# Kernel optimization log

Measured on AMD Instinct MI355X. Metric: run time of the kernel, lower is better.

The kernel has to match this reference:

```python
import jax, jax.numpy as jnp
import numpy as np

B, D, S, H, L = 256, 7, 32, 512, 128  # batch, tree depth, n_symbols, hidden_size, latent_size
N = 2 ** D - 1  # nodes in complete binary tree, heap order (children of i are 2i+1, 2i+2)


def _xavier(key, shape):
    lim = float(np.sqrt(6.0 / (shape[0] + shape[1])))
    return jax.random.uniform(key, shape, jnp.float32, -lim, lim)


def setup_inputs():
    key = jax.random.key(0)
    ks = jax.random.split(key, 18)
    return {
        'symbols': jax.random.randint(ks[0], (B, N), 0, S, dtype=jnp.int32),
        'eps': jax.random.normal(ks[1], (B, L), jnp.float32),
        # Encoder GRU221: gate order [r, z, n], input weights act on one-hot symbol, hidden weights on cat(h_l, h_r)
        'ewi': _xavier(ks[2], (3 * H, S)),
        'ebi': jax.random.uniform(ks[3], (3 * H,), jnp.float32, -0.05, 0.05),
        'ewh': _xavier(ks[4], (3 * H, 2 * H)),
        'ebh': jax.random.uniform(ks[5], (3 * H,), jnp.float32, -0.05, 0.05),
        'h2mu_w': _xavier(ks[6], (L, H)),
        'h2mu_b': jax.random.uniform(ks[7], (L,), jnp.float32, -0.05, 0.05),
        'h2lv_w': _xavier(ks[8], (L, H)),
        'h2lv_b': jax.random.uniform(ks[9], (L,), jnp.float32, -0.05, 0.05),
        # Decoder
        'z2h_w': _xavier(ks[10], (H, L)),
        'z2h_b': jax.random.uniform(ks[11], (H,), jnp.float32, -0.05, 0.05),
        'h2o_w': _xavier(ks[12], (S, H)),
        'h2o_b': jax.random.uniform(ks[13], (S,), jnp.float32, -0.05, 0.05),
        # Decoder GRU122: gate order [r, z, n], each gate has 2H outputs (left/right child)
        'dwi': _xavier(ks[14], (6 * H, S)),
        'dbi': jax.random.uniform(ks[15], (6 * H,), jnp.float32, -0.05, 0.05),
        'dwh': _xavier(ks[16], (6 * H, H)),
        'dbh': jax.random.uniform(ks[17], (6 * H,), jnp.float32, -0.05, 0.05),
    }


def _hvae_forward(symbols, eps, ewi, ebi, ewh, ebh, h2mu_w, h2mu_b, h2lv_w, h2lv_b,
                  z2h_w, z2h_b, h2o_w, h2o_b, dwi, dbi, dwh, dbh):
    x_all = jax.nn.one_hot(symbols, S, dtype=jnp.float32)  # [B, N, S] node targets

    # ---- Encoder: GRU221 applied bottom-up, one batched step per tree level ----
    h = jnp.zeros((B, 2 ** D, H), jnp.float32)  # (absent) children of the deepest level
    for d in range(D - 1, -1, -1):
        n_d = 2 ** d
        x = x_all[:, n_d - 1: 2 * n_d - 1]       # [B, n_d, S] level-d symbols (heap order)
        hl, hr = h[:, 0::2], h[:, 1::2]           # [B, n_d, H] left/right child hiddens
        hcat = jnp.concatenate([hl, hr], axis=-1)
        gi = x @ ewi.T + ebi                       # [B, n_d, 3H]
        gh = hcat @ ewh.T + ebh
        r = jax.nn.sigmoid(gi[..., :H] + gh[..., :H])
        zg = jax.nn.sigmoid(gi[..., H:2 * H] + gh[..., H:2 * H])
        n = jnp.tanh(gi[..., 2 * H:] + r * gh[..., 2 * H:])
        h = (1.0 - zg) * n + zg * (hl + hr) * 0.5
    root = h[:, 0]                                 # [B, H]
    mu = root @ h2mu_w.T + h2mu_b                  # [B, L]
    logvar = root @ h2lv_w.T + h2lv_b
    zlat = mu + eps * jnp.exp(0.5 * logvar)        # reparameterized sample

    # ---- Decoder: GRU122 applied top-down, one batched step per tree level ----
    hidden = (zlat @ z2h_w.T + z2h_b)[:, None, :]  # [B, 1, H] root hidden
    preds = []
    for d in range(D):
        pred = hidden @ h2o_w.T + h2o_b            # [B, 2^d, S]
        preds.append(pred)
        if d < D - 1:
            a = jax.nn.softmax(pred, axis=-1)
            gi = a @ dwi.T + dbi                    # [B, 2^d, 6H]
            gh = hidden @ dwh.T + dbh
            r = jax.nn.sigmoid(gi[..., :2 * H] + gh[..., :2 * H])
            zg = jax.nn.sigmoid(gi[..., 2 * H:4 * H] + gh[..., 2 * H:4 * H])
            n = jnp.tanh(gi[..., 4 * H:] + r * gh[..., 4 * H:])
            dh = jnp.concatenate([hidden, hidden], axis=-1)  # h.repeat(1,1,2)
            out = (1.0 - zg) * n + zg * dh          # [B, 2^d, 2H]
            # torch.split -> (left, right); interleave as next level's hiddens (heap order)
            hidden = jnp.stack([out[..., :H], out[..., H:]], axis=2).reshape(B, 2 ** (d + 1), H)
    preds = jnp.concatenate(preds, axis=1)          # [B, N, S] per-node logits, level order
    return mu, logvar, preds


def reference(symbols, eps, ewi, ebi, ewh, ebh, h2mu_w, h2mu_b, h2lv_w, h2lv_b,
              z2h_w, z2h_b, h2o_w, h2o_b, dwi, dbi, dwh, dbh):
    return _hvae_forward(symbols, eps, ewi, ebi, ewh, ebh, h2mu_w, h2mu_b, h2lv_w, h2lv_b,
                         z2h_w, z2h_b, h2o_w, h2o_b, dwi, dbi, dwh, dbh)
```

## Files before the change

kernel.cpp:

```cpp
#include <hip/hip_runtime.h>
#include <hip/hip_bf16.h>

typedef unsigned short u16;
typedef unsigned int u32;
typedef __attribute__((ext_vector_type(8))) short short8;
typedef __attribute__((ext_vector_type(4))) float f32x4;

#define WAITV(N) asm volatile("s_waitcnt vmcnt(" #N ")" ::: "memory")

__device__ __forceinline__ float sigmoidf_(float x) { return 1.0f / (1.0f + expf(-x)); }
__device__ __forceinline__ float fsig(float x) {
    return __builtin_amdgcn_rcpf(1.0f + __expf(-x));
}
__device__ __forceinline__ float ftanh(float x) {
    x = fminf(fmaxf(x, -15.0f), 15.0f);
    float t = __expf(2.0f * x);
    return (t - 1.0f) * __builtin_amdgcn_rcpf(t + 1.0f);
}

__device__ __forceinline__ float bf2f(u16 u) {
    union { u32 i; float f; } v; v.i = ((u32)u) << 16; return v.f;
}
__device__ __forceinline__ u16 f2bf(float f) {
    union { float f; u32 i; } v; v.f = f;
    u32 lsb = (v.i >> 16) & 1u;
    v.i += 0x7fffu + lsb;
    return (u16)(v.i >> 16);
}

__device__ __forceinline__ void gload16(const u16* g, u16* l) {
    __builtin_amdgcn_global_load_lds(
        (const __attribute__((address_space(1))) u32*)g,
        (__attribute__((address_space(3))) u32*)l, 16, 0, 0);
}

__global__ __launch_bounds__(256) void prep(
    const float* __restrict__ ewh, const float* __restrict__ dwh,
    const float* __restrict__ dwi, const float* __restrict__ ewi,
    const float* __restrict__ h2o_w, const int* __restrict__ symbols,
    const float* __restrict__ ebi, const float* __restrict__ ebh,
    u16* __restrict__ ewh_b, u16* __restrict__ dwh_b, u16* __restrict__ dwi_b,
    u16* __restrict__ ewi_b, u16* __restrict__ wo_b, u16* __restrict__ oneh,
    u16* __restrict__ ltab)
{
    int idx = blockIdx.x * 256 + threadIdx.x;
    if (idx < 1572864) { ewh_b[idx] = f2bf(ewh[idx]); return; }
    idx -= 1572864;
    if (idx < 1572864) { dwh_b[idx] = f2bf(dwh[idx]); return; }
    idx -= 1572864;
    if (idx < 98304) { dwi_b[idx] = f2bf(dwi[idx]); return; }
    idx -= 98304;
    if (idx < 49152) { ewi_b[idx] = f2bf(ewi[idx]); return; }
    idx -= 49152;
    if (idx < 16384) { wo_b[idx] = f2bf(h2o_w[idx]); return; }
    idx -= 16384;
    if (idx < 1040384) {
        int col = idx & 31, row = idx >> 5;
        oneh[idx] = (col == symbols[row]) ? (u16)0x3F80 : (u16)0;
        return;
    }
    idx -= 1040384;
    if (idx < 16384) {
        int c = idx & 511, sym = idx >> 9;
        float r = sigmoidf_(ewi[c * 32 + sym]          + ebi[c]        + ebh[c]);
        float z = sigmoidf_(ewi[(512 + c) * 32 + sym]  + ebi[512 + c]  + ebh[512 + c]);
        float n = tanhf(    ewi[(1024 + c) * 32 + sym] + ebi[1024 + c] + r * ebh[1024 + c]);
        ltab[idx] = f2bf((1.0f - z) * n);
    }
}

template<int RF, bool LEAF>
__global__ __launch_bounds__(256, 2) void enc_tile(
    const u16* __restrict__ A, const u16* __restrict__ W,
    const u16* __restrict__ oneh, const u16* __restrict__ Wi,
    const u16* __restrict__ tab, const int* __restrict__ symbols,
    const float* __restrict__ ebi, const float* __restrict__ ebh,
    u16* __restrict__ hout, int dlog, int node_base)
{
    constexpr int BM = RF * 32;
    constexpr int NCA = BM / 64;
    constexpr int NS = 32;
    __shared__ alignas(16) u16 Als[2][BM * 32];
    __shared__ alignas(16) u16 Bls[2][192 * 32];
    const int tid  = threadIdx.x;
    const int lane = tid & 63;
    const int wid  = tid >> 6;
    const int wr = wid >> 1, wc = wid & 1;
    const int lr = lane & 15, lk = lane >> 4;
    const int m0 = blockIdx.x * BM;
    const int c0 = blockIdx.y * 64;
    const int mask = (1 << dlog) - 1;

    size_t a_goff[NCA]; int a_loff[NCA];
    int symL[NCA], symR[NCA];
#pragma unroll
    for (int j = 0; j < NCA; ++j) {
        int a = wid * NCA + j;
        int r_ = a * 16 + (lane >> 2);
        int kps = (lane & 3) ^ ((r_ >> 1) & 3);
        a_loff[j] = a * 512 + lane * 8;
        if constexpr (LEAF) {
            int rg = m0 + r_;
            int b_ = rg >> dlog, jj = rg & mask;
            int cbase = b_ * 127 + 2 * (node_base + jj) + 1;
            symL[j] = symbols[cbase];
            symR[j] = symbols[cbase + 1];
            a_goff[j] = kps * 8;
        } else {
            a_goff[j] = (size_t)(m0 + r_) * 1024 + kps * 8;
            symL[j] = symR[j] = 0;
        }
    }
    size_t b_goff[3]; int b_loff[3];
#pragma unroll
    for (int j = 0; j < 3; ++j) {
        int b = wid * 3 + j;
        int rr = b * 16 + (lane >> 2);
        int kps = (lane & 3) ^ ((rr >> 1) & 3);
        int grow = (rr >> 6) * 512 + c0 + (rr & 63);
        b_goff[j] = (size_t)grow * 1024 + kps * 8;
        b_loff[j] = b * 512 + lane * 8;
    }
    int a_roff[RF];
#pragma unroll
    for (int i = 0; i < RF; ++i) {
        int row = wr * (RF * 16) + i * 16 + lr;
        a_roff[i] = row * 32 + (lk ^ ((row >> 1) & 3)) * 8;
    }
    int b_roff[3][2];
#pragma unroll
    for (int s = 0; s < 3; ++s)
#pragma unroll
        for (int cf = 0; cf < 2; ++cf) {
            int row = s * 64 + wc * 32 + cf * 16 + lr;
            b_roff[s][cf] = row * 32 + (lk ^ ((row >> 1) & 3)) * 8;
        }

    f32x4 acc[4][2][RF];
#pragma unroll
    for (int s = 0; s < 4; ++s)
#pragma unroll
        for (int cf = 0; cf < 2; ++cf)
#pragma unroll
            for (int i = 0; i < RF; ++i) acc[s][cf][i] = (f32x4){0.f, 0.f, 0.f, 0.f};

    auto issue = [&](int stg) {
        const int buf = stg & 1;
        const int nk = stg * 32;
#pragma unroll
        for (int j = 0; j < NCA; ++j) {
            if constexpr (LEAF) {
                const u16* src = (nk < 512)
                    ? tab + (size_t)symL[j] * 512 + nk + a_goff[j]
                    : tab + (size_t)symR[j] * 512 + (nk - 512) + a_goff[j];
                gload16(src, &Als[buf][a_loff[j]]);
            } else {
                gload16(A + a_goff[j] + nk, &Als[buf][a_loff[j]]);
            }
        }
#pragma unroll
        for (int j = 0; j < 3; ++j) gload16(W + b_goff[j] + nk, &Bls[buf][b_loff[j]]);
    };
    auto compute = [&](int buf) {
        short8 a[RF];
#pragma unroll
        for (int i = 0; i < RF; ++i)
            a[i] = *reinterpret_cast<const short8*>(&Als[buf][a_roff[i]]);
#pragma unroll
        for (int s = 0; s < 3; ++s)
#pragma unroll
            for (int cf = 0; cf < 2; ++cf) {
                short8 b = *reinterpret_cast<const short8*>(&Bls[buf][b_roff[s][cf]]);
#pragma unroll
                for (int i = 0; i < RF; ++i)
                    acc[s][cf][i] = __builtin_amdgcn_mfma_f32_16x16x32_bf16(b, a[i], acc[s][cf][i], 0, 0, 0);
            }
    };

    issue(0);
    WAITV(0);
    __builtin_amdgcn_s_barrier();
    for (int t = 0; t < NS - 1; ++t) {
        issue(t + 1);
        compute(t & 1);
        WAITV(0);
        __builtin_amdgcn_s_barrier();
    }
    compute((NS - 1) & 1);

    {
        short8 oh[RF];
#pragma unroll
        for (int i = 0; i < RF; ++i) {
            int m = m0 + wr * (RF * 16) + i * 16 + lr;
            int b_ = m >> dlog, j_ = m & mask;
            oh[i] = *reinterpret_cast<const short8*>(
                oneh + (size_t)(b_ * 127 + node_base + j_) * 32 + lk * 8);
        }
#pragma unroll
        for (int s = 0; s < 3; ++s) {
            const int d = (s == 2) ? 3 : s;
#pragma unroll
            for (int cf = 0; cf < 2; ++cf) {
                short8 wb = *reinterpret_cast<const short8*>(
                    Wi + (size_t)(s * 512 + c0 + wc * 32 + cf * 16 + lr) * 32 + lk * 8);
#pragma unroll
                for (int i = 0; i < RF; ++i)
                    acc[d][cf][i] = __builtin_amdgcn_mfma_f32_16x16x32_bf16(wb, oh[i], acc[d][cf][i], 0, 0, 0);
            }
        }
    }

    float4 ebr4[2], ebz4[2], ebin4[2], ebhn4[2];
    int cb[2];
#pragma unroll
    for (int cf = 0; cf < 2; ++cf) {
        cb[cf] = c0 + wc * 32 + cf * 16 + lk * 4;
        float4 bi0 = *reinterpret_cast<const float4*>(ebi + cb[cf]);
        float4 bh0 = *reinterpret_cast<const float4*>(ebh + cb[cf]);
        float4 bi1 = *reinterpret_cast<const float4*>(ebi + 512 + cb[cf]);
        float4 bh1 = *reinterpret_cast<const float4*>(ebh + 512 + cb[cf]);
        ebr4[cf] = make_float4(bi0.x + bh0.x, bi0.y + bh0.y, bi0.z + bh0.z, bi0.w + bh0.w);
        ebz4[cf] = make_float4(bi1.x + bh1.x, bi1.y + bh1.y, bi1.z + bh1.z, bi1.w + bh1.w);
        ebin4[cf] = *reinterpret_cast<const float4*>(ebi + 1024 + cb[cf]);
        ebhn4[cf] = *reinterpret_cast<const float4*>(ebh + 1024 + cb[cf]);
    }
#pragma unroll
    for (int i = 0; i < RF; ++i) {
        int m = m0 + wr * (RF * 16) + i * 16 + lr;
        int symLm = 0, symRm = 0;
        if constexpr (LEAF) {
            int b_ = m >> dlog, jj = m & mask;
            int cbase_ = b_ * 127 + 2 * (node_base + jj) + 1;
            symLm = symbols[cbase_];
            symRm = symbols[cbase_ + 1];
        }
#pragma unroll
        for (int cf = 0; cf < 2; ++cf) {
            ushort4 hl4, hr4;
            if constexpr (LEAF) {
                hl4 = *reinterpret_cast<const ushort4*>(tab + (size_t)symLm * 512 + cb[cf]);
                hr4 = *reinterpret_cast<const ushort4*>(tab + (size_t)symRm * 512 + cb[cf]);
            } else {
                hl4 = *reinterpret_cast<const ushort4*>(A + (size_t)m * 1024 + cb[cf]);
                hr4 = *reinterpret_cast<const ushort4*>(A + (size_t)m * 1024 + 512 + cb[cf]);
            }
            const float eb_r[4] = {ebr4[cf].x, ebr4[cf].y, ebr4[cf].z, ebr4[cf].w};
            const float eb_z[4] = {ebz4[cf].x, ebz4[cf].y, ebz4[cf].z, ebz4[cf].w};
            const float eb_in[4] = {ebin4[cf].x, ebin4[cf].y, ebin4[cf].z, ebin4[cf].w};
            const float eb_hn[4] = {ebhn4[cf].x, ebhn4[cf].y, ebhn4[cf].z, ebhn4[cf].w};
            const u16 hlv[4] = {hl4.x, hl4.y, hl4.z, hl4.w};
            const u16 hrv[4] = {hr4.x, hr4.y, hr4.z, hr4.w};
            ushort4 outv;
            u16* ov = reinterpret_cast<u16*>(&outv);
#pragma unroll
            for (int r = 0; r < 4; ++r) {
                float rr_ = fsig(acc[0][cf][i][r] + eb_r[r]);
                float zz  = fsig(acc[1][cf][i][r] + eb_z[r]);
                float nn  = ftanh(acc[3][cf][i][r] + eb_in[r] + rr_ * (acc[2][cf][i][r] + eb_hn[r]));
                float hm = (bf2f(hlv[r]) + bf2f(hrv[r])) * 0.5f;
                ov[r] = f2bf((1.0f - zz) * nn + zz * hm);
            }
            *reinterpret_cast<ushort4*>(hout + (size_t)m * 512 + cb[cf]) = outv;
        }
    }
}

__global__ __launch_bounds__(256) void midf(
    const u16* __restrict__ root, const float* __restrict__ h2mu_w,
    const float* __restrict__ h2mu_b, const float* __restrict__ h2lv_w,
    const float* __restrict__ h2lv_b, const float* __restrict__ eps,
    const float* __restrict__ z2h_w, const float* __restrict__ z2h_b,
    float* __restrict__ out_mu, float* __restrict__ out_lv,
    u16* __restrict__ hidden)
{
    int b = blockIdx.x, t = threadIdx.x;
    __shared__ float rs[512];
    __shared__ float zl[128];
    rs[t]       = bf2f(root[(size_t)b * 512 + t]);
    rs[t + 256] = bf2f(root[(size_t)b * 512 + t + 256]);
    __syncthreads();
    const float* w = (t < 128) ? (h2mu_w + (size_t)t * 512) : (h2lv_w + (size_t)(t - 128) * 512);
    float acc = 0.0f;
    for (int k = 0; k < 512; ++k) acc += rs[k] * w[k];
    acc += (t < 128) ? h2mu_b[t] : h2lv_b[t - 128];
    __shared__ float vals[256];
    vals[t] = acc;
    __syncthreads();
    if (t < 128) {
        float mu = vals[t], lv = vals[t + 128];
        zl[t] = mu + eps[b * 128 + t] * expf(0.5f * lv);
        out_mu[b * 128 + t] = mu;
        out_lv[b * 128 + t] = lv;
    }
    __syncthreads();
    for (int c = t; c < 512; c += 256) {
        float a2 = z2h_b[c];
        const float* wz = z2h_w + (size_t)c * 128;
        for (int k = 0; k < 128; ++k) a2 += zl[k] * wz[k];
        hidden[(size_t)b * 512 + c] = f2bf(a2);
    }
}

__global__ __launch_bounds__(256) void pred_mfma(
    const u16* __restrict__ hidden, const u16* __restrict__ Wo,
    const float* __restrict__ h2o_b, float* __restrict__ preds_out,
    int dlog, int node_base)
{
    const int lane = threadIdx.x & 63;
    const int wid  = threadIdx.x >> 6;
    const int lr = lane & 15, lk = lane >> 4;
    const int m0 = blockIdx.x * 64 + wid * 16;

    f32x4 acc0 = (f32x4){0.f, 0.f, 0.f, 0.f};
    f32x4 acc1 = (f32x4){0.f, 0.f, 0.f, 0.f};
    const u16* Arow = hidden + (size_t)(m0 + lr) * 512 + lk * 8;
    const u16* B0 = Wo + (size_t)lr * 512 + lk * 8;
    const u16* B1 = Wo + (size_t)(16 + lr) * 512 + lk * 8;
#pragma unroll
    for (int k0 = 0; k0 < 512; k0 += 32) {
        short8 a  = *reinterpret_cast<const short8*>(Arow + k0);
        short8 b0 = *reinterpret_cast<const short8*>(B0 + k0);
        short8 b1 = *reinterpret_cast<const short8*>(B1 + k0);
        acc0 = __builtin_amdgcn_mfma_f32_16x16x32_bf16(b0, a, acc0, 0, 0, 0);
        acc1 = __builtin_amdgcn_mfma_f32_16x16x32_bf16(b1, a, acc1, 0, 0, 0);
    }
    float4 bb0 = *reinterpret_cast<const float4*>(h2o_b + lk * 4);
    float4 bb1 = *reinterpret_cast<const float4*>(h2o_b + 16 + lk * 4);
    float p0[4], p1[4];
    p0[0] = acc0[0] + bb0.x; p0[1] = acc0[1] + bb0.y; p0[2] = acc0[2] + bb0.z; p0[3] = acc0[3] + bb0.w;
    p1[0] = acc1[0] + bb1.x; p1[1] = acc1[1] + bb1.y; p1[2] = acc1[2] + bb1.z; p1[3] = acc1[3] + bb1.w;
    int m = m0 + lr;
    int b_ = m >> dlog, j_ = m & ((1 << dlog) - 1);
    size_t o = (size_t)(b_ * 127 + node_base + j_) * 32;
    *reinterpret_cast<float4*>(preds_out + o + lk * 4)      = make_float4(p0[0], p0[1], p0[2], p0[3]);
    *reinterpret_cast<float4*>(preds_out + o + 16 + lk * 4) = make_float4(p1[0], p1[1], p1[2], p1[3]);
}

template<int RF>
__global__ __launch_bounds__(256, 2) void dec_tile(
    const u16* __restrict__ Hin, const u16* __restrict__ Wh,
    const u16* __restrict__ Wi, const u16* __restrict__ Wo,
    const float* __restrict__ dbh, const float* __restrict__ dbi,
    const float* __restrict__ h2o_b, u16* __restrict__ Hout,
    float* __restrict__ preds_out, int dlog, int node_base)
{
    constexpr int BM = RF * 32;
    constexpr int NCA = BM / 64;
    constexpr int NS = 16;
    __shared__ alignas(16) u16 Als[2][BM * 32];
    __shared__ alignas(16) u16 Bls[2][192 * 32];
    const int tid  = threadIdx.x;
    const int lane = tid & 63;
    const int wid  = tid >> 6;
    const int wr = wid >> 1, wc = wid & 1;
    const int lr = lane & 15, lk = lane >> 4;
    const int m0 = blockIdx.x * BM;
    const int c0 = blockIdx.y * 64;
    const int mask = (1 << dlog) - 1;

    size_t a_goff[NCA]; int a_loff[NCA];
#pragma unroll
    for (int j = 0; j < NCA; ++j) {
        int a = wid * NCA + j;
        int r_ = a * 16 + (lane >> 2);
        int kps = (lane & 3) ^ ((r_ >> 1) & 3);
        a_goff[j] = (size_t)(m0 + r_) * 512 + kps * 8;
        a_loff[j] = a * 512 + lane * 8;
    }
    size_t b_goff[3]; int b_loff[3];
#pragma unroll
    for (int j = 0; j < 3; ++j) {
        int b = wid * 3 + j;
        int rr = b * 16 + (lane >> 2);
        int kps = (lane & 3) ^ ((rr >> 1) & 3);
        int grow = (rr >> 6) * 1024 + c0 + (rr & 63);
        b_goff[j] = (size_t)grow * 512 + kps * 8;
        b_loff[j] = b * 512 + lane * 8;
    }
    int a_roff[RF];
#pragma unroll
    for (int i = 0; i < RF; ++i) {
        int row = wr * (RF * 16) + i * 16 + lr;
        a_roff[i] = row * 32 + (lk ^ ((row >> 1) & 3)) * 8;
    }
    int b_roff[3][2];
#pragma unroll
    for (int s = 0; s < 3; ++s)
#pragma unroll
        for (int cf = 0; cf < 2; ++cf) {
            int row = s * 64 + wc * 32 + cf * 16 + lr;
            b_roff[s][cf] = row * 32 + (lk ^ ((row >> 1) & 3)) * 8;
        }

    f32x4 acc[4][2][RF];
#pragma unroll
    for (int s = 0; s < 4; ++s)
#pragma unroll
        for (int cf = 0; cf < 2; ++cf)
#pragma unroll
            for (int i = 0; i < RF; ++i) acc[s][cf][i] = (f32x4){0.f, 0.f, 0.f, 0.f};
    f32x4 accp[2][RF];
#pragma unroll
    for (int cf = 0; cf < 2; ++cf)
#pragma unroll
        for (int i = 0; i < RF; ++i) accp[cf][i] = (f32x4){0.f, 0.f, 0.f, 0.f};

    auto issue = [&](int stg) {
        const int buf = stg & 1;
        const int nk = stg * 32;
#pragma unroll
        for (int j = 0; j < NCA; ++j) gload16(Hin + a_goff[j] + nk, &Als[buf][a_loff[j]]);
#pragma unroll
        for (int j = 0; j < 3; ++j) gload16(Wh + b_goff[j] + nk, &Bls[buf][b_loff[j]]);
    };
    auto compute = [&](int buf, int t) {
        short8 a[RF];
#pragma unroll
        for (int i = 0; i < RF; ++i)
            a[i] = *reinterpret_cast<const short8*>(&Als[buf][a_roff[i]]);
#pragma unroll
        for (int s = 0; s < 3; ++s)
#pragma unroll
            for (int cf = 0; cf < 2; ++cf) {
                short8 b = *reinterpret_cast<const short8*>(&Bls[buf][b_roff[s][cf]]);
#pragma unroll
                for (int i = 0; i < RF; ++i)
                    acc[s][cf][i] = __builtin_amdgcn_mfma_f32_16x16x32_bf16(b, a[i], acc[s][cf][i], 0, 0, 0);
            }
#pragma unroll
        for (int cf = 0; cf < 2; ++cf) {
            short8 wo = *reinterpret_cast<const short8*>(
                Wo + (size_t)(cf * 16 + lr) * 512 + t * 32 + lk * 8);
#pragma unroll
            for (int i = 0; i < RF; ++i)
                accp[cf][i] = __builtin_amdgcn_mfma_f32_16x16x32_bf16(wo, a[i], accp[cf][i], 0, 0, 0);
        }
    };

    issue(0);
    WAITV(0);
    __builtin_amdgcn_s_barrier();
    for (int t = 0; t < NS - 1; ++t) {
        issue(t + 1);
        compute(t & 1, t);
        WAITV(0);
        __builtin_amdgcn_s_barrier();
    }
    compute((NS - 1) & 1, NS - 1);

    u16* aLds = &Als[0][0];
    {
        float4 bb0 = *reinterpret_cast<const float4*>(h2o_b + lk * 4);
        float4 bb1 = *reinterpret_cast<const float4*>(h2o_b + 16 + lk * 4);
#pragma unroll
        for (int i = 0; i < RF; ++i) {
            float p0[4], p1[4];
            p0[0] = accp[0][i][0] + bb0.x; p0[1] = accp[0][i][1] + bb0.y;
            p0[2] = accp[0][i][2] + bb0.z; p0[3] = accp[0][i][3] + bb0.w;
            p1[0] = accp[1][i][0] + bb1.x; p1[1] = accp[1][i][1] + bb1.y;
            p1[2] = accp[1][i][2] + bb1.z; p1[3] = accp[1][i][3] + bb1.w;
            float mx = fmaxf(fmaxf(fmaxf(p0[0], p0[1]), fmaxf(p0[2], p0[3])),
                             fmaxf(fmaxf(p1[0], p1[1]), fmaxf(p1[2], p1[3])));
            mx = fmaxf(mx, __shfl_xor(mx, 16));
            mx = fmaxf(mx, __shfl_xor(mx, 32));
            float e0[4], e1[4], s = 0.0f;
#pragma unroll
            for (int r = 0; r < 4; ++r) {
                e0[r] = __expf(p0[r] - mx); e1[r] = __expf(p1[r] - mx);
                s += e0[r] + e1[r];
            }
            s += __shfl_xor(s, 16);
            s += __shfl_xor(s, 32);
            int mloc = wr * (RF * 16) + i * 16 + lr;
            int m = m0 + mloc;
            if (blockIdx.y == 0 && wc == 0) {
                int b_ = m >> dlog, j_ = m & mask;
                size_t o = (size_t)(b_ * 127 + node_base + j_) * 32;
                *reinterpret_cast<float4*>(preds_out + o + lk * 4)      = make_float4(p0[0], p0[1], p0[2], p0[3]);
                *reinterpret_cast<float4*>(preds_out + o + 16 + lk * 4) = make_float4(p1[0], p1[1], p1[2], p1[3]);
            }
            if (wc == 0) {
                float inv = __builtin_amdgcn_rcpf(s);
                ushort4 a0, a1;
                u16* av0 = reinterpret_cast<u16*>(&a0);
                u16* av1 = reinterpret_cast<u16*>(&a1);
#pragma unroll
                for (int r = 0; r < 4; ++r) { av0[r] = f2bf(e0[r] * inv); av1[r] = f2bf(e1[r] * inv); }
                *reinterpret_cast<ushort4*>(aLds + mloc * 32 + lk * 4)      = a0;
                *reinterpret_cast<ushort4*>(aLds + mloc * 32 + 16 + lk * 4) = a1;
            }
        }
    }
    __builtin_amdgcn_s_barrier();

#pragma unroll
    for (int i = 0; i < RF; ++i) {
        int mloc = wr * (RF * 16) + i * 16 + lr;
        short8 aw = *reinterpret_cast<const short8*>(aLds + mloc * 32 + lk * 8);
#pragma unroll
        for (int s = 0; s < 3; ++s) {
            const int d = (s == 2) ? 3 : s;
#pragma unroll
            for (int cf = 0; cf < 2; ++cf) {
                short8 b = *reinterpret_cast<const short8*>(
                    Wi + (size_t)(s * 1024 + c0 + wc * 32 + cf * 16 + lr) * 32 + lk * 8);
                acc[d][cf][i] = __builtin_amdgcn_mfma_f32_16x16x32_bf16(b, aw, acc[d][cf][i], 0, 0, 0);
            }
        }
    }

    float4 br4[2], bz4[2], bin4[2], bhn4[2];
    int cb[2];
#pragma unroll
    for (int cf = 0; cf < 2; ++cf) {
        cb[cf] = c0 + wc * 32 + cf * 16 + lk * 4;
        float4 h0 = *reinterpret_cast<const float4*>(dbh + cb[cf]);
        float4 i0 = *reinterpret_cast<const float4*>(dbi + cb[cf]);
        float4 h1 = *reinterpret_cast<const float4*>(dbh + 1024 + cb[cf]);
        float4 i1 = *reinterpret_cast<const float4*>(dbi + 1024 + cb[cf]);
        br4[cf] = make_float4(h0.x + i0.x, h0.y + i0.y, h0.z + i0.z, h0.w + i0.w);
        bz4[cf] = make_float4(h1.x + i1.x, h1.y + i1.y, h1.z + i1.z, h1.w + i1.w);
        bin4[cf] = *reinterpret_cast<const float4*>(dbi + 2048 + cb[cf]);
        bhn4[cf] = *reinterpret_cast<const float4*>(dbh + 2048 + cb[cf]);
    }
#pragma unroll
    for (int i = 0; i < RF; ++i) {
        int m = m0 + wr * (RF * 16) + i * 16 + lr;
#pragma unroll
        for (int cf = 0; cf < 2; ++cf) {
            ushort4 hid4 = *reinterpret_cast<const ushort4*>(Hin + (size_t)m * 512 + (cb[cf] & 511));
            const float b_r[4] = {br4[cf].x, br4[cf].y, br4[cf].z, br4[cf].w};
            const float b_z[4] = {bz4[cf].x, bz4[cf].y, bz4[cf].z, bz4[cf].w};
            const float b_in[4] = {bin4[cf].x, bin4[cf].y, bin4[cf].z, bin4[cf].w};
            const float b_hn[4] = {bhn4[cf].x, bhn4[cf].y, bhn4[cf].z, bhn4[cf].w};
            const u16 hv[4] = {hid4.x, hid4.y, hid4.z, hid4.w};
            ushort4 outv;
            u16* ov = reinterpret_cast<u16*>(&outv);
#pragma unroll
            for (int r = 0; r < 4; ++r) {
                float rr_ = fsig(acc[0][cf][i][r] + b_r[r]);
                float zz  = fsig(acc[1][cf][i][r] + b_z[r]);
                float nn  = ftanh(acc[3][cf][i][r] + b_in[r] + rr_ * (acc[2][cf][i][r] + b_hn[r]));
                ov[r] = f2bf((1.0f - zz) * nn + zz * bf2f(hv[r]));
            }
            *reinterpret_cast<ushort4*>(Hout + (size_t)m * 1024 + cb[cf]) = outv;
        }
    }
}

extern "C" void kernel_launch(void* const* d_in, const int* in_sizes, int n_in,
                              void* d_out, int out_size, void* d_ws, size_t ws_size,
                              hipStream_t stream) {
    const int*   symbols = (const int*)  d_in[0];
    const float* eps     = (const float*)d_in[1];
    const float* ewi     = (const float*)d_in[2];
    const float* ebi     = (const float*)d_in[3];
    const float* ewh     = (const float*)d_in[4];
    const float* ebh     = (const float*)d_in[5];
    const float* h2mu_w  = (const float*)d_in[6];
    const float* h2mu_b  = (const float*)d_in[7];
    const float* h2lv_w  = (const float*)d_in[8];
    const float* h2lv_b  = (const float*)d_in[9];
    const float* z2h_w   = (const float*)d_in[10];
    const float* z2h_b   = (const float*)d_in[11];
    const float* h2o_w   = (const float*)d_in[12];
    const float* h2o_b   = (const float*)d_in[13];
    const float* dwi     = (const float*)d_in[14];
    const float* dbi     = (const float*)d_in[15];
    const float* dwh     = (const float*)d_in[16];
    const float* dbh     = (const float*)d_in[17];

    float* out    = (float*)d_out;
    float* out_mu = out;
    float* out_lv = out + 256 * 128;
    float* out_pr = out + 2 * 256 * 128;

    u16* bufL  = (u16*)d_ws;
    u16* bufS  = bufL  + (size_t)16384 * 512;
    u16* ewh_b = bufS  + (size_t)8192 * 512;
    u16* dwh_b = ewh_b + (size_t)1536 * 1024;
    u16* dwi_b = dwh_b + (size_t)3072 * 512;
    u16* ewi_b = dwi_b + (size_t)3072 * 32;
    u16* wo_b  = ewi_b + (size_t)1536 * 32;
    u16* ltab  = wo_b  + (size_t)32 * 512;
    u16* oneh  = ltab  + (size_t)32 * 512;

    prep<<<(4366336 + 255) / 256, 256, 0, stream>>>(
        ewh, dwh, dwi, ewi, h2o_w, symbols, ebi, ebh,
        ewh_b, dwh_b, dwi_b, ewi_b, wo_b, oneh, ltab);

    enc_tile<4, true><<<dim3(64, 8), 256, 0, stream>>>(
        nullptr, ewh_b, oneh, ewi_b, ltab, symbols, ebi, ebh, bufS, 5, 31);
    const u16* src = bufS;
    u16*       dst = bufL;
    for (int d = 4; d >= 0; --d) {
        int M = 256 << d;
        if (M >= 4096)
            enc_tile<4, false><<<dim3(M / 128, 8), 256, 0, stream>>>(
                src, ewh_b, oneh, ewi_b, ltab, symbols, ebi, ebh, dst, d, (1 << d) - 1);
        else
            enc_tile<2, false><<<dim3(M / 64, 8), 256, 0, stream>>>(
                src, ewh_b, oneh, ewi_b, ltab, symbols, ebi, ebh, dst, d, (1 << d) - 1);
        const u16* t = src; src = dst; dst = (u16*)t;
    }
    midf<<<256, 256, 0, stream>>>(src, h2mu_w, h2mu_b, h2lv_w, h2lv_b, eps,
                                  z2h_w, z2h_b, out_mu, out_lv, bufL);

    const u16* hsrc = bufL;
    u16*       hdst = bufS;
    for (int d = 0; d < 6; ++d) {
        int M = 256 << d;
        if (M >= 4096)
            dec_tile<4><<<dim3(M / 128, 16), 256, 0, stream>>>(
                hsrc, dwh_b, dwi_b, wo_b, dbh, dbi, h2o_b, hdst, out_pr, d, (1 << d) - 1);
        else
            dec_tile<2><<<dim3(M / 64, 16), 256, 0, stream>>>(
                hsrc, dwh_b, dwi_b, wo_b, dbh, dbi, h2o_b, hdst, out_pr, d, (1 << d) - 1);
        const u16* t = hsrc; hsrc = hdst; hdst = (u16*)t;
    }
    pred_mfma<<<16384 / 64, 256, 0, stream>>>(hsrc, wo_b, h2o_b, out_pr, 6, 63);
}
```

Baseline: 347.8 us.

## Vectorize prep conversion, split-K final prediction, restrict decoder logits to one wave column

```diff
diff --git a/kernel.cpp b/kernel.cpp
--- a/kernel.cpp
+++ b/kernel.cpp
@@ -32,6 +32,13 @@
     __builtin_amdgcn_global_load_lds(
         (const __attribute__((address_space(1))) u32*)g,
         (__attribute__((address_space(3))) u32*)l, 16, 0, 0);
+}
+
+__device__ __forceinline__ ushort4 cvt4(const float* src) {
+    float4 v = *reinterpret_cast<const float4*>(src);
+    ushort4 o;
+    o.x = f2bf(v.x); o.y = f2bf(v.y); o.z = f2bf(v.z); o.w = f2bf(v.w);
+    return o;
 }
 
 __global__ __launch_bounds__(256) void prep(
@@ -43,29 +50,42 @@
     u16* __restrict__ ewi_b, u16* __restrict__ wo_b, u16* __restrict__ oneh,
     u16* __restrict__ ltab)
 {
-    int idx = blockIdx.x * 256 + threadIdx.x;
-    if (idx < 1572864) { ewh_b[idx] = f2bf(ewh[idx]); return; }
+    int idx = (blockIdx.x * 256 + threadIdx.x) * 4;
+    if (idx < 1572864) { *reinterpret_cast<ushort4*>(ewh_b + idx) = cvt4(ewh + idx); return; }
     idx -= 1572864;
-    if (idx < 1572864) { dwh_b[idx] = f2bf(dwh[idx]); return; }
+    if (idx < 1572864) { *reinterpret_cast<ushort4*>(dwh_b + idx) = cvt4(dwh + idx); return; }
     idx -= 1572864;
-    if (idx < 98304) { dwi_b[idx] = f2bf(dwi[idx]); return; }
+    if (idx < 98304) { *reinterpret_cast<ushort4*>(dwi_b + idx) = cvt4(dwi + idx); return; }
     idx -= 98304;
-    if (idx < 49152) { ewi_b[idx] = f2bf(ewi[idx]); return; }
+    if (idx < 49152) { *reinterpret_cast<ushort4*>(ewi_b + idx) = cvt4(ewi + idx); return; }
     idx -= 49152;
-    if (idx < 16384) { wo_b[idx] = f2bf(h2o_w[idx]); return; }
+    if (idx < 16384) { *reinterpret_cast<ushort4*>(wo_b + idx) = cvt4(h2o_w + idx); return; }
     idx -= 16384;
     if (idx < 1040384) {
-        int col = idx & 31, row = idx >> 5;
-        oneh[idx] = (col == symbols[row]) ? (u16)0x3F80 : (u16)0;
+        int row = idx >> 5, col0 = idx & 31;
+        int sym = symbols[row];
+        ushort4 o;
+        o.x = (col0 + 0 == sym) ? (u16)0x3F80 : (u16)0;
+        o.y = (col0 + 1 == sym) ? (u16)0x3F80 : (u16)0;
+        o.z = (col0 + 2 == sym) ? (u16)0x3F80 : (u16)0;
+        o.w = (col0 + 3 == sym) ? (u16)0x3F80 : (u16)0;
+        *reinterpret_cast<ushort4*>(oneh + idx) = o;
         return;
     }
     idx -= 1040384;
     if (idx < 16384) {
-        int c = idx & 511, sym = idx >> 9;
-        float r = sigmoidf_(ewi[c * 32 + sym]          + ebi[c]        + ebh[c]);
-        float z = sigmoidf_(ewi[(512 + c) * 32 + sym]  + ebi[512 + c]  + ebh[512 + c]);
-        float n = tanhf(    ewi[(1024 + c) * 32 + sym] + ebi[1024 + c] + r * ebh[1024 + c]);
-        ltab[idx] = f2bf((1.0f - z) * n);
+        int sym = idx >> 9, c0 = idx & 511;
+        ushort4 o;
+        u16* ov = reinterpret_cast<u16*>(&o);
+#pragma unroll
+        for (int r = 0; r < 4; ++r) {
+            int c = c0 + r;
+            float rr = sigmoidf_(ewi[c * 32 + sym]          + ebi[c]        + ebh[c]);
+            float zz = sigmoidf_(ewi[(512 + c) * 32 + sym]  + ebi[512 + c]  + ebh[512 + c]);
+            float nn = tanhf(    ewi[(1024 + c) * 32 + sym] + ebi[1024 + c] + rr * ebh[1024 + c]);
+            ov[r] = f2bf((1.0f - zz) * nn);
+        }
+        *reinterpret_cast<ushort4*>(ltab + idx) = o;
     }
 }
 
@@ -302,39 +322,46 @@
     }
 }
 
-__global__ __launch_bounds__(256) void pred_mfma(
+__global__ __launch_bounds__(256) void pred_final(
     const u16* __restrict__ hidden, const u16* __restrict__ Wo,
-    const float* __restrict__ h2o_b, float* __restrict__ preds_out,
-    int dlog, int node_base)
+    const float* __restrict__ h2o_b, float* __restrict__ preds_out)
 {
-    const int lane = threadIdx.x & 63;
-    const int wid  = threadIdx.x >> 6;
+    __shared__ float pbuf[4][32][17];
+    const int tid = threadIdx.x;
+    const int lane = tid & 63;
+    const int w = tid >> 6;
     const int lr = lane & 15, lk = lane >> 4;
-    const int m0 = blockIdx.x * 64 + wid * 16;
+    const int m0 = blockIdx.x * 16;
 
     f32x4 acc0 = (f32x4){0.f, 0.f, 0.f, 0.f};
     f32x4 acc1 = (f32x4){0.f, 0.f, 0.f, 0.f};
-    const u16* Arow = hidden + (size_t)(m0 + lr) * 512 + lk * 8;
-    const u16* B0 = Wo + (size_t)lr * 512 + lk * 8;
-    const u16* B1 = Wo + (size_t)(16 + lr) * 512 + lk * 8;
-#pragma unroll
-    for (int k0 = 0; k0 < 512; k0 += 32) {
+    const u16* Arow = hidden + (size_t)(m0 + lr) * 512 + w * 128 + lk * 8;
+    const u16* B0 = Wo + (size_t)lr * 512 + w * 128 + lk * 8;
+    const u16* B1 = Wo + (size_t)(16 + lr) * 512 + w * 128 + lk * 8;
+#pragma unroll
+    for (int k0 = 0; k0 < 128; k0 += 32) {
         short8 a  = *reinterpret_cast<const short8*>(Arow + k0);
         short8 b0 = *reinterpret_cast<const short8*>(B0 + k0);
         short8 b1 = *reinterpret_cast<const short8*>(B1 + k0);
         acc0 = __builtin_amdgcn_mfma_f32_16x16x32_bf16(b0, a, acc0, 0, 0, 0);
         acc1 = __builtin_amdgcn_mfma_f32_16x16x32_bf16(b1, a, acc1, 0, 0, 0);
     }
-    float4 bb0 = *reinterpret_cast<const float4*>(h2o_b + lk * 4);
-    float4 bb1 = *reinterpret_cast<const float4*>(h2o_b + 16 + lk * 4);
-    float p0[4], p1[4];
-    p0[0] = acc0[0] + bb0.x; p0[1] = acc0[1] + bb0.y; p0[2] = acc0[2] + bb0.z; p0[3] = acc0[3] + bb0.w;
-    p1[0] = acc1[0] + bb1.x; p1[1] = acc1[1] + bb1.y; p1[2] = acc1[2] + bb1.z; p1[3] = acc1[3] + bb1.w;
-    int m = m0 + lr;
-    int b_ = m >> dlog, j_ = m & ((1 << dlog) - 1);
-    size_t o = (size_t)(b_ * 127 + node_base + j_) * 32;
-    *reinterpret_cast<float4*>(preds_out + o + lk * 4)      = make_float4(p0[0], p0[1], p0[2], p0[3]);
-    *reinterpret_cast<float4*>(preds_out + o + 16 + lk * 4) = make_float4(p1[0], p1[1], p1[2], p1[3]);
+#pragma unroll
+    for (int r = 0; r < 4; ++r) {
+        pbuf[w][lk * 4 + r][lr]      = acc0[r];
+        pbuf[w][16 + lk * 4 + r][lr] = acc1[r];
+    }
+    __syncthreads();
+#pragma unroll
+    for (int it = 0; it < 2; ++it) {
+        int o = tid + it * 256;
+        int mloc = o >> 5, sym = o & 31;
+        float p = pbuf[0][sym][mloc] + pbuf[1][sym][mloc]
+                + pbuf[2][sym][mloc] + pbuf[3][sym][mloc] + h2o_b[sym];
+        int m = m0 + mloc;
+        int b_ = m >> 6, j_ = m & 63;
+        preds_out[(size_t)(b_ * 127 + 63 + j_) * 32 + sym] = p;
+    }
 }
 
 template<int RF>
@@ -428,13 +455,15 @@
                 for (int i = 0; i < RF; ++i)
                     acc[s][cf][i] = __builtin_amdgcn_mfma_f32_16x16x32_bf16(b, a[i], acc[s][cf][i], 0, 0, 0);
             }
-#pragma unroll
-        for (int cf = 0; cf < 2; ++cf) {
-            short8 wo = *reinterpret_cast<const short8*>(
-                Wo + (size_t)(cf * 16 + lr) * 512 + t * 32 + lk * 8);
-#pragma unroll
-            for (int i = 0; i < RF; ++i)
-                accp[cf][i] = __builtin_amdgcn_mfma_f32_16x16x32_bf16(wo, a[i], accp[cf][i], 0, 0, 0);
+        if (wc == 0) {
+#pragma unroll
+            for (int cf = 0; cf < 2; ++cf) {
+                short8 wo = *reinterpret_cast<const short8*>(
+                    Wo + (size_t)(cf * 16 + lr) * 512 + t * 32 + lk * 8);
+#pragma unroll
+                for (int i = 0; i < RF; ++i)
+                    accp[cf][i] = __builtin_amdgcn_mfma_f32_16x16x32_bf16(wo, a[i], accp[cf][i], 0, 0, 0);
+            }
         }
     };
 
@@ -450,7 +479,7 @@
     compute((NS - 1) & 1, NS - 1);
 
     u16* aLds = &Als[0][0];
-    {
+    if (wc == 0) {
         float4 bb0 = *reinterpret_cast<const float4*>(h2o_b + lk * 4);
         float4 bb1 = *reinterpret_cast<const float4*>(h2o_b + 16 + lk * 4);
 #pragma unroll
@@ -474,22 +503,20 @@
             s += __shfl_xor(s, 32);
             int mloc = wr * (RF * 16) + i * 16 + lr;
             int m = m0 + mloc;
-            if (blockIdx.y == 0 && wc == 0) {
+            if (blockIdx.y == 0) {
                 int b_ = m >> dlog, j_ = m & mask;
                 size_t o = (size_t)(b_ * 127 + node_base + j_) * 32;
                 *reinterpret_cast<float4*>(preds_out + o + lk * 4)      = make_float4(p0[0], p0[1], p0[2], p0[3]);
                 *reinterpret_cast<float4*>(preds_out + o + 16 + lk * 4) = make_float4(p1[0], p1[1], p1[2], p1[3]);
             }
-            if (wc == 0) {
-                float inv = __builtin_amdgcn_rcpf(s);
-                ushort4 a0, a1;
-                u16* av0 = reinterpret_cast<u16*>(&a0);
-                u16* av1 = reinterpret_cast<u16*>(&a1);
-#pragma unroll
-                for (int r = 0; r < 4; ++r) { av0[r] = f2bf(e0[r] * inv); av1[r] = f2bf(e1[r] * inv); }
-                *reinterpret_cast<ushort4*>(aLds + mloc * 32 + lk * 4)      = a0;
-                *reinterpret_cast<ushort4*>(aLds + mloc * 32 + 16 + lk * 4) = a1;
-            }
+            float inv = __builtin_amdgcn_rcpf(s);
+            ushort4 a0, a1;
+            u16* av0 = reinterpret_cast<u16*>(&a0);
+            u16* av1 = reinterpret_cast<u16*>(&a1);
+#pragma unroll
+            for (int r = 0; r < 4; ++r) { av0[r] = f2bf(e0[r] * inv); av1[r] = f2bf(e1[r] * inv); }
+            *reinterpret_cast<ushort4*>(aLds + mloc * 32 + lk * 4)      = a0;
+            *reinterpret_cast<ushort4*>(aLds + mloc * 32 + 16 + lk * 4) = a1;
         }
     }
     __builtin_amdgcn_s_barrier();
@@ -586,7 +613,7 @@
     u16* ltab  = wo_b  + (size_t)32 * 512;
     u16* oneh  = ltab  + (size_t)32 * 512;
 
-    prep<<<(4366336 + 255) / 256, 256, 0, stream>>>(
+    prep<<<(1091584 + 255) / 256, 256, 0, stream>>>(
         ewh, dwh, dwi, ewi, h2o_w, symbols, ebi, ebh,
         ewh_b, dwh_b, dwi_b, ewi_b, wo_b, oneh, ltab);
 
@@ -619,5 +646,5 @@
                 hsrc, dwh_b, dwi_b, wo_b, dbh, dbi, h2o_b, hdst, out_pr, d, (1 << d) - 1);
         const u16* t = hsrc; hsrc = hdst; hdst = (u16*)t;
     }
-    pred_mfma<<<16384 / 64, 256, 0, stream>>>(hsrc, wo_b, h2o_b, out_pr, 6, 63);
-}
+    pred_final<<<16384 / 16, 256, 0, stream>>>(hsrc, wo_b, h2o_b, out_pr);
+}
```

Measured after the change: 336.9 us. 1.03x faster.
